# Kernel tuning notes

Hardware: AMD Instinct MI355X
Metric: run time of the kernel (lower is better)

The kernel has to match this reference:

```python
import jax, jax.numpy as jnp
import numpy as np

B, C, H, W, M = 16, 4, 64, 64, 2048  # frames, coils, image grid, samples/frame


def setup_inputs() -> dict:
    key = jax.random.key(0)
    k1, k2, k3 = jax.random.split(key, 3)
    x_real = jax.random.normal(k1, (B, C, H, W), dtype=jnp.float32)
    x_imag = jax.random.normal(k2, (B, C, H, W), dtype=jnp.float32)
    # non-uniform k-space trajectory, radians in [-pi, pi), per frame
    traj = (jax.random.uniform(k3, (B, M, 2), dtype=jnp.float32) - 0.5) * (2.0 * np.pi)
    return {"x_real": x_real, "x_imag": x_imag, "traj": traj}


def _nufft_type2(x, traj):
    """Exact type-2 NUFFT (image -> non-uniform k-space), the math cufinufft approximates.
    x: [B, C, H, W] complex64, traj: [B, M, 2] float32 (radians).
    Returns y: [B, C, M] complex64 with y[b,c,m] = sum_n x[b,c,n] * exp(-i * t_m . n).
    """
    b, c, h, w = x.shape
    gy = jnp.arange(h, dtype=jnp.float32) - h // 2
    gx = jnp.arange(w, dtype=jnp.float32) - w // 2
    coords = jnp.stack(jnp.meshgrid(gy, gx, indexing="ij"), axis=-1).reshape(-1, 2)  # [N, 2]
    phase = jnp.einsum("bmd,nd->bmn", traj, coords)  # [B, M, N]
    e = jnp.exp(-1j * phase)  # complex64 DFT matrix per frame
    y = jnp.einsum("bmn,bcn->bcm", e, x.reshape(b, c, -1))
    return y


def reference(x_real, x_imag, traj):
    x = x_real + 1j * x_imag  # [B, C, H, W] complex64
    y = _nufft_type2(x, traj)  # [B, C, M] complex64
    # return real/imag stacked so output is a real float32 tensor [B, C, M, 2]
    return jnp.stack([y.real, y.imag], axis=-1)
```

## Files before the change

### kernel.cpp

```cpp
#include <hip/hip_runtime.h>
#include <hip/hip_fp16.h>
#include <math.h>

#define B_ 16
#define C_ 4
#define M_ 2048

typedef short bf16x8 __attribute__((ext_vector_type(8)));
typedef float f32x4 __attribute__((ext_vector_type(4)));

__device__ inline unsigned short f2bf(float f) {
  union { float f; unsigned u; } v; v.f = f;
  unsigned r = v.u + 0x7fffu + ((v.u >> 16) & 1u);
  return (unsigned short)(r >> 16);
}

__device__ inline bf16x8 pack2(float4 a, float4 b) {
  bf16x8 r;
  r[0] = (short)f2bf(a.x); r[1] = (short)f2bf(a.y);
  r[2] = (short)f2bf(a.z); r[3] = (short)f2bf(a.w);
  r[4] = (short)f2bf(b.x); r[5] = (short)f2bf(b.y);
  r[6] = (short)f2bf(b.z); r[7] = (short)f2bf(b.w);
  return r;
}
__device__ inline float4 neg4(float4 a) { return make_float4(-a.x, -a.y, -a.z, -a.w); }
__device__ inline float4 sel4(int c, float4 a, float4 b) {
  return make_float4(c ? a.x : b.x, c ? a.y : b.y, c ? a.z : b.z, c ? a.w : b.w);
}

__global__ __launch_bounds__(512) void nufft_kernel(const float* __restrict__ xr,
                                                    const float* __restrict__ xi,
                                                    const float* __restrict__ traj,
                                                    float* __restrict__ out) {
  const int b = blockIdx.x >> 4;
  const int m0 = (blockIdx.x & 15) * 128;
  const int tid = threadIdx.x;
  const int lane = tid & 63;
  const int wave = tid >> 6;
  const int c = wave & 3;
  const int g = wave >> 2;
  const int col = lane & 15;
  const int quad = lane >> 4;

  __shared__ __align__(16) unsigned short ExS[128][136];
  __shared__ __align__(16) __half2 EyS[128][65];
  __shared__ __align__(16) float ypart[2][4][128][2];

  bf16x8 bfrag[4][4];
  {
    const int ri = col & 1;
    const float* rb = xr + (size_t)((b * 4 + c) * 64) * 64;
    const float* ib = xi + (size_t)((b * 4 + c) * 64) * 64;
    const int ja = quad * 8;
    const int jb = 32 + quad * 8;
#pragma unroll
    for (int nt = 0; nt < 4; ++nt) {
      const int i = g * 32 + nt * 8 + (col >> 1);
      const float* rrow = rb + i * 64;
      const float* irow = ib + i * 64;
      const float4 r0 = *(const float4*)(rrow + ja);
      const float4 r1 = *(const float4*)(rrow + ja + 4);
      const float4 r2 = *(const float4*)(rrow + jb);
      const float4 r3 = *(const float4*)(rrow + jb + 4);
      const float4 i0 = *(const float4*)(irow + ja);
      const float4 i1 = *(const float4*)(irow + ja + 4);
      const float4 i2 = *(const float4*)(irow + jb);
      const float4 i3 = *(const float4*)(irow + jb + 4);
      bfrag[nt][0] = pack2(sel4(ri, i0, r0), sel4(ri, i1, r1));
      bfrag[nt][1] = pack2(sel4(ri, i2, r2), sel4(ri, i3, r3));
      bfrag[nt][2] = pack2(sel4(ri, r0, neg4(i0)), sel4(ri, r1, neg4(i1)));
      bfrag[nt][3] = pack2(sel4(ri, r2, neg4(i2)), sel4(ri, r3, neg4(i3)));
    }
  }

  {
    const int mh = tid >> 2;
    const int j0 = (tid & 3) * 16;
    const int mg = m0 + mh;
    const float ky = traj[((size_t)b * M_ + mg) * 2 + 0];
    const float kx = traj[((size_t)b * M_ + mg) * 2 + 1];
    float sa, ca, su, cu;
    sincosf(kx * (float)(j0 - 32), &sa, &ca);
    float vr = ca, vi = -sa;
    sincosf(kx, &su, &cu);
    const float ur = cu, ui = -su;
#pragma unroll
    for (int s = 0; s < 16; ++s) {
      ExS[mh][j0 + s] = f2bf(vr);
      ExS[mh][64 + j0 + s] = f2bf(vi);
      const float nvr = fmaf(vr, ur, -(vi * ui));
      const float nvi = fmaf(vr, ui, vi * ur);
      vr = nvr; vi = nvi;
    }
    sincosf(ky * (float)(j0 - 32), &sa, &ca);
    float wr = ca, wi = -sa;
    sincosf(ky, &su, &cu);
    const float pr = cu, pi = -su;
#pragma unroll
    for (int s = 0; s < 16; ++s) {
      EyS[mh][j0 + s] = __floats2half2_rn(wr, wi);
      const float nwr = fmaf(wr, pr, -(wi * pi));
      const float nwi = fmaf(wr, pi, wi * pr);
      wr = nwr; wi = nwi;
    }
  }
  __syncthreads();

  const int ri = col & 1;
  const int ih = col >> 1;

#pragma unroll 1
  for (int s = 0; s < 8; ++s) {
    bf16x8 af[4];
#pragma unroll
    for (int ks = 0; ks < 4; ++ks)
      af[ks] = *(const bf16x8*)(&ExS[s * 16 + col][ks * 32 + quad * 8]);

    f32x4 acc[4];
#pragma unroll
    for (int nt = 0; nt < 4; ++nt) acc[nt] = (f32x4){0.f, 0.f, 0.f, 0.f};

#pragma unroll
    for (int ks = 0; ks < 4; ++ks)
#pragma unroll
      for (int nt = 0; nt < 4; ++nt)
        acc[nt] = __builtin_amdgcn_mfma_f32_16x16x32_bf16(af[ks], bfrag[nt][ks], acc[nt], 0, 0, 0);

    float yr[4], yi[4];
#pragma unroll
    for (int r = 0; r < 4; ++r) {
      const int m_loc = s * 16 + quad * 4 + r;
      float ar = 0.f, ai = 0.f;
#pragma unroll
      for (int nt = 0; nt < 4; ++nt) {
        const __half2 e = EyS[m_loc][g * 32 + nt * 8 + ih];
        const float er = __low2float(e), ei = __high2float(e);
        const float p = acc[nt][r];
        const float ca = ri ? -ei : er;
        const float cb = ri ? er : ei;
        ar = fmaf(ca, p, ar);
        ai = fmaf(cb, p, ai);
      }
      yr[r] = ar; yi[r] = ai;
    }

#pragma unroll
    for (int mk = 1; mk <= 8; mk <<= 1) {
#pragma unroll
      for (int r = 0; r < 4; ++r) {
        yr[r] += __shfl_xor(yr[r], mk, 64);
        yi[r] += __shfl_xor(yi[r], mk, 64);
      }
    }

    if (col < 8) {
      const int ro = col & 1;
      const int rr = col >> 1;
      const float v0 = ro ? yi[0] : yr[0];
      const float v1 = ro ? yi[1] : yr[1];
      const float v2 = ro ? yi[2] : yr[2];
      const float v3 = ro ? yi[3] : yr[3];
      const float v = (rr == 0) ? v0 : (rr == 1) ? v1 : (rr == 2) ? v2 : v3;
      ypart[g][c][s * 16 + quad * 4 + rr][ro] = v;
    }
  }

  __syncthreads();

  {
    const int cc = tid >> 7;
    const int m = tid & 127;
    const float2 a0 = *(const float2*)&ypart[0][cc][m][0];
    const float2 a1 = *(const float2*)&ypart[1][cc][m][0];
    float2 v;
    v.x = a0.x + a1.x;
    v.y = a0.y + a1.y;
    *(float2*)&out[((size_t)(b * 4 + cc) * M_ + m0 + m) * 2] = v;
  }
}

extern "C" void kernel_launch(void* const* d_in, const int* in_sizes, int n_in,
                              void* d_out, int out_size, void* d_ws, size_t ws_size,
                              hipStream_t stream) {
  const float* xr = (const float*)d_in[0];
  const float* xi = (const float*)d_in[1];
  const float* traj = (const float*)d_in[2];
  float* out = (float*)d_out;
  (void)d_ws; (void)ws_size;

  nufft_kernel<<<B_ * 16, 512, 0, stream>>>(xr, xi, traj, out);
}
```

Measured before the change: 73.32 us.

## Transpose MFMA output and compute y-phase factors in registers, dropping EyS table

Swaps the MFMA operand order so each lane holds accumulators for a single sample m across four image rows. The y-direction phase factors are then generated in registers with fast sincos and a rotation recurrence, rather than read from a half2 shared-memory table. This removes the EyS table build and its LDS reads, and shrinks the cross-lane reduction from four xor-shuffle stages over eight values to two stages over two values. It also switches the x-direction phase setup to the fast __sincosf intrinsic, which gives up some accuracy on large arguments.

```diff
diff --git a/kernel.cpp b/kernel.cpp
--- a/kernel.cpp
+++ b/kernel.cpp
@@ -43,8 +43,7 @@
   const int quad = lane >> 4;
 
   __shared__ __align__(16) unsigned short ExS[128][136];
-  __shared__ __align__(16) __half2 EyS[128][65];
-  __shared__ __align__(16) float ypart[2][4][128][2];
+  __shared__ __align__(16) float2 ypart[2][4][128];
 
   bf16x8 bfrag[4][4];
   {
@@ -76,13 +75,11 @@
   {
     const int mh = tid >> 2;
     const int j0 = (tid & 3) * 16;
-    const int mg = m0 + mh;
-    const float ky = traj[((size_t)b * M_ + mg) * 2 + 0];
-    const float kx = traj[((size_t)b * M_ + mg) * 2 + 1];
+    const float kx = traj[((size_t)b * M_ + m0 + mh) * 2 + 1];
     float sa, ca, su, cu;
-    sincosf(kx * (float)(j0 - 32), &sa, &ca);
+    __sincosf(kx * (float)(j0 - 32), &sa, &ca);
     float vr = ca, vi = -sa;
-    sincosf(kx, &su, &cu);
+    __sincosf(kx, &su, &cu);
     const float ur = cu, ui = -su;
 #pragma unroll
     for (int s = 0; s < 16; ++s) {
@@ -92,25 +89,13 @@
       const float nvi = fmaf(vr, ui, vi * ur);
       vr = nvr; vi = nvi;
     }
-    sincosf(ky * (float)(j0 - 32), &sa, &ca);
-    float wr = ca, wi = -sa;
-    sincosf(ky, &su, &cu);
-    const float pr = cu, pi = -su;
-#pragma unroll
-    for (int s = 0; s < 16; ++s) {
-      EyS[mh][j0 + s] = __floats2half2_rn(wr, wi);
-      const float nwr = fmaf(wr, pr, -(wi * pi));
-      const float nwi = fmaf(wr, pi, wi * pr);
-      wr = nwr; wi = nwi;
-    }
   }
   __syncthreads();
 
-  const int ri = col & 1;
-  const int ih = col >> 1;
-
 #pragma unroll 1
   for (int s = 0; s < 8; ++s) {
+    const float ky = traj[((size_t)b * M_ + m0 + s * 16 + col) * 2 + 0];
+
     bf16x8 af[4];
 #pragma unroll
     for (int ks = 0; ks < 4; ++ks)
@@ -124,45 +109,33 @@
     for (int ks = 0; ks < 4; ++ks)
 #pragma unroll
       for (int nt = 0; nt < 4; ++nt)
-        acc[nt] = __builtin_amdgcn_mfma_f32_16x16x32_bf16(af[ks], bfrag[nt][ks], acc[nt], 0, 0, 0);
+        acc[nt] = __builtin_amdgcn_mfma_f32_16x16x32_bf16(bfrag[nt][ks], af[ks], acc[nt], 0, 0, 0);
 
-    float yr[4], yi[4];
+    float su, cu, s8, c8, sb, cb;
+    __sincosf(ky, &su, &cu);
+    __sincosf(8.0f * ky, &s8, &c8);
+    __sincosf(ky * (float)(g * 32 + quad * 2 - 32), &sb, &cb);
+    float er = cb, ei = -sb;
+    float yr = 0.f, yi = 0.f;
 #pragma unroll
-    for (int r = 0; r < 4; ++r) {
-      const int m_loc = s * 16 + quad * 4 + r;
-      float ar = 0.f, ai = 0.f;
-#pragma unroll
-      for (int nt = 0; nt < 4; ++nt) {
-        const __half2 e = EyS[m_loc][g * 32 + nt * 8 + ih];
-        const float er = __low2float(e), ei = __high2float(e);
-        const float p = acc[nt][r];
-        const float ca = ri ? -ei : er;
-        const float cb = ri ? er : ei;
-        ar = fmaf(ca, p, ar);
-        ai = fmaf(cb, p, ai);
-      }
-      yr[r] = ar; yi[r] = ai;
+    for (int nt = 0; nt < 4; ++nt) {
+      const float er1 = fmaf(er, cu, ei * su);
+      const float ei1 = fmaf(ei, cu, -(er * su));
+      yr = fmaf(er, acc[nt][0], fmaf(-ei, acc[nt][1], yr));
+      yi = fmaf(ei, acc[nt][0], fmaf(er, acc[nt][1], yi));
+      yr = fmaf(er1, acc[nt][2], fmaf(-ei1, acc[nt][3], yr));
+      yi = fmaf(ei1, acc[nt][2], fmaf(er1, acc[nt][3], yi));
+      const float ern = fmaf(er, c8, ei * s8);
+      const float ein = fmaf(ei, c8, -(er * s8));
+      er = ern; ei = ein;
     }
 
-#pragma unroll
-    for (int mk = 1; mk <= 8; mk <<= 1) {
-#pragma unroll
-      for (int r = 0; r < 4; ++r) {
-        yr[r] += __shfl_xor(yr[r], mk, 64);
-        yi[r] += __shfl_xor(yi[r], mk, 64);
-      }
-    }
+    yr += __shfl_xor(yr, 16, 64);
+    yr += __shfl_xor(yr, 32, 64);
+    yi += __shfl_xor(yi, 16, 64);
+    yi += __shfl_xor(yi, 32, 64);
 
-    if (col < 8) {
-      const int ro = col & 1;
-      const int rr = col >> 1;
-      const float v0 = ro ? yi[0] : yr[0];
-      const float v1 = ro ? yi[1] : yr[1];
-      const float v2 = ro ? yi[2] : yr[2];
-      const float v3 = ro ? yi[3] : yr[3];
-      const float v = (rr == 0) ? v0 : (rr == 1) ? v1 : (rr == 2) ? v2 : v3;
-      ypart[g][c][s * 16 + quad * 4 + rr][ro] = v;
-    }
+    if (quad == 0) ypart[g][c][s * 16 + col] = make_float2(yr, yi);
   }
 
   __syncthreads();
@@ -170,8 +143,8 @@
   {
     const int cc = tid >> 7;
     const int m = tid & 127;
-    const float2 a0 = *(const float2*)&ypart[0][cc][m][0];
-    const float2 a1 = *(const float2*)&ypart[1][cc][m][0];
+    const float2 a0 = ypart[0][cc][m];
+    const float2 a1 = ypart[1][cc][m];
     float2 v;
     v.x = a0.x + a1.x;
     v.y = a0.y + a1.y;
```

Result: faster. 68.72 us (-6.3%).
